# Kernel tuning notes

Hardware: AMD Instinct MI355X
Metric: run time of the kernel (lower is better)

The kernel has to match this reference:

```python
import jax, jax.numpy as jnp
import numpy as np

B_, K_, D_, L_, N_, R_ = 4, 4, 96, 2048, 16, 6
C_ = R_ + 2 * N_  # 38


def setup_inputs() -> dict:
    key = jax.random.key(0)
    ks = jax.random.split(key, 6)
    scale = 0.05  # keep projections in a realistic range (like 1/sqrt(fan_in) init)
    return {
        "xs": jax.random.normal(ks[0], (B_, K_, D_, L_), dtype=jnp.float32),
        "A_logs": jax.random.uniform(ks[1], (K_ * D_, N_), dtype=jnp.float32),
        "Ds": jax.random.normal(ks[2], (K_ * D_,), dtype=jnp.float32),
        "dt_projs_weight": jax.random.normal(ks[3], (K_, D_, R_), dtype=jnp.float32) * scale,
        "dt_projs_bias": jax.random.normal(ks[4], (K_, D_), dtype=jnp.float32) * scale,
        "x_proj_weight": jax.random.normal(ks[5], (K_, C_, D_), dtype=jnp.float32) * scale,
    }


def reference(xs, A_logs, Ds, dt_projs_weight, dt_projs_bias, x_proj_weight):
    B, K, D, L = xs.shape
    N = A_logs.shape[1]
    R = dt_projs_weight.shape[2]

    xs = xs.astype(jnp.float32)  # force_fp32=True

    # project x -> (delta, B, C):  [B,K,C,L]
    x_dbl = jnp.einsum("bkdl,kcd->bkcl", xs, x_proj_weight)
    dts, Bs, Cs = x_dbl[:, :, :R], x_dbl[:, :, R:R + N], x_dbl[:, :, R + N:]
    # dt low-rank -> per-channel delta: [B,K,D,L]
    dts = jnp.einsum("bkrl,kdr->bkdl", dts, dt_projs_weight)

    A = -jnp.exp(A_logs.astype(jnp.float32)).reshape(K, D, N)  # [K,D,N]
    Dskd = Ds.astype(jnp.float32).reshape(K, D)

    # delta_softplus with delta_bias
    delta = jax.nn.softplus(dts + dt_projs_bias.astype(jnp.float32)[None, :, :, None])

    # discretization: deltaA [B,K,D,L,N], deltaB_u [B,K,D,L,N]
    dA = jnp.exp(delta[..., None] * A[None, :, :, None, :])
    dBu = jnp.einsum("bkdl,bknl,bkdl->bkdln", delta, Bs, xs)

    # linear recurrence h_t = dA_t * h_{t-1} + dBu_t via parallel associative scan over L
    def combine(e1, e2):
        a1, b1 = e1
        a2, b2 = e2
        return a1 * a2, a2 * b1 + b2

    _, hs = jax.lax.associative_scan(combine, (dA, dBu), axis=3)  # hs: [B,K,D,L,N]

    # y_t = C_t . h_t + D * x_t
    y = jnp.einsum("bkdln,bknl->bkdl", hs, Cs) + Dskd[None, :, :, None] * xs
    return y.astype(jnp.float32)  # [B,K,D,L]
```

## Files before the change

kernel.cpp:

```cpp
#include <hip/hip_runtime.h>
#include <hip/hip_fp16.h>
#include <math.h>

#define B_ 4
#define K_ 4
#define D_ 96
#define L_ 2048
#define N_ 16
#define R_ 6
#define C_ 38

__device__ __forceinline__ float softplus_f(float x) {
    return fmaxf(x, 0.f) + __logf(1.f + __expf(-fabsf(x)));
}

#if __has_builtin(__builtin_amdgcn_exp2f)
__device__ __forceinline__ float exp2_fast(float x) { return __builtin_amdgcn_exp2f(x); }
#else
__device__ __forceinline__ float exp2_fast(float x) { return __expf(0.6931471805599453f * x); }
#endif

__device__ __forceinline__ float h2f(const uint4& v, int e) {
    return __half2float(((const __half*)&v)[e]);
}


__global__ __launch_bounds__(256) void proj_kernel(
    const float* __restrict__ xs, const float* __restrict__ xpw,
    uint4* __restrict__ BCc, float* __restrict__ dts_ws)
{
    __shared__ float sWt[D_][24];
    const int bk = blockIdx.x;
    const int k = bk & 3;
    const int cg = blockIdx.z;
    const int tid = threadIdx.x;
    const int c0 = (cg == 0) ? 0 : (R_ + N_);
    const int nr = (cg == 0) ? 22 : 16;

    for (int i = tid; i < nr * D_; i += 256) {
        const int r = i / D_, dd = i % D_;
        sWt[dd][r] = xpw[(k * C_ + c0 + r) * D_ + dd];
    }
    __syncthreads();

    const int l = blockIdx.y * 256 + tid;
    const float* Xl = xs + (size_t)bk * D_ * L_ + l;
    const int i8 = l & 7, t8 = l >> 3;
    uint4* BCb = BCc + ((size_t)bk * 8 + i8) * 4 * 256 + t8;

    if (cg == 0) {
        float acc[22];
#pragma unroll
        for (int r = 0; r < 22; ++r) acc[r] = 0.f;
#pragma unroll
        for (int d = 0; d < D_; ++d) {
            const float xv = Xl[d * L_];
            float wv[24];
#pragma unroll
            for (int q = 0; q < 6; ++q)
                *(float4*)&wv[q * 4] = *(const float4*)&sWt[d][q * 4];
#pragma unroll
            for (int r = 0; r < 22; ++r) acc[r] = fmaf(wv[r], xv, acc[r]);
        }
#pragma unroll
        for (int r = 0; r < R_; ++r)
            dts_ws[((size_t)bk * R_ + r) * L_ + l] = acc[r];
        union { __half h[8]; uint4 v; } p0, p1;
#pragma unroll
        for (int e = 0; e < 8; ++e) {
            p0.h[e] = __float2half(acc[6 + e]);
            p1.h[e] = __float2half(acc[14 + e]);
        }
        BCb[0 * 256] = p0.v;
        BCb[1 * 256] = p1.v;
    } else {
        float acc[16];
#pragma unroll
        for (int r = 0; r < 16; ++r) acc[r] = 0.f;
#pragma unroll
        for (int d = 0; d < D_; ++d) {
            const float xv = Xl[d * L_];
            float wv[16];
#pragma unroll
            for (int q = 0; q < 4; ++q)
                *(float4*)&wv[q * 4] = *(const float4*)&sWt[d][q * 4];
#pragma unroll
            for (int r = 0; r < 16; ++r) acc[r] = fmaf(wv[r], xv, acc[r]);
        }
        union { __half h[8]; uint4 v; } p0, p1;
#pragma unroll
        for (int e = 0; e < 8; ++e) {
            p0.h[e] = __float2half(acc[e]);
            p1.h[e] = __float2half(acc[8 + e]);
        }
        BCb[2 * 256] = p0.v;
        BCb[3 * 256] = p1.v;
    }
}

__global__ __launch_bounds__(512) void scan_kernel(
    const float* __restrict__ xs, const float* __restrict__ A_logs,
    const float* __restrict__ Ds, const float* __restrict__ dtw,
    const float* __restrict__ dtb, const float* __restrict__ dts_ws,
    const uint4* __restrict__ BCc, float* __restrict__ out)
{
    __shared__ float sAw[8][8];
    __shared__ float sBw[8][8];
    __shared__ float sy[256][9];

    const int bkd = blockIdx.x;
    const int d = bkd % D_;
    const int bk = bkd / D_;
    const int k = bk & 3;
    const int kd = k * D_ + d;
    const int tid = threadIdx.x;
    const int g = tid >> 8;
    const int t = tid & 255;
    const int lane = tid & 63;
    const int gw = tid >> 6;

    const uint4* BC = BCc + (size_t)bk * 8 * 4 * 256;
    const int jB = g, jC = 2 + g;

    const float4* xv4 = (const float4*)(xs + (size_t)bkd * L_);
    const float4 xa = xv4[t * 2], xb = xv4[t * 2 + 1];
    float x[8] = {xa.x, xa.y, xa.z, xa.w, xb.x, xb.y, xb.z, xb.w};

    float del[8];
    const float bias = dtb[kd];
#pragma unroll
    for (int j = 0; j < 8; ++j) del[j] = bias;
    const float* w2 = dtw + (size_t)kd * R_;
    const float4* dts4 = (const float4*)(dts_ws + (size_t)bk * R_ * L_);
#pragma unroll
    for (int r = 0; r < R_; ++r) {
        const float wr = w2[r];
        const float4 t0 = dts4[r * (L_ / 4) + t * 2];
        const float4 t1 = dts4[r * (L_ / 4) + t * 2 + 1];
        del[0] = fmaf(wr, t0.x, del[0]); del[1] = fmaf(wr, t0.y, del[1]);
        del[2] = fmaf(wr, t0.z, del[2]); del[3] = fmaf(wr, t0.w, del[3]);
        del[4] = fmaf(wr, t1.x, del[4]); del[5] = fmaf(wr, t1.y, del[5]);
        del[6] = fmaf(wr, t1.z, del[6]); del[7] = fmaf(wr, t1.w, del[7]);
    }
#pragma unroll
    for (int j = 0; j < 8; ++j) del[j] = softplus_f(del[j]);

    float A2[8];
    const float* Ap = A_logs + (size_t)kd * N_ + g * 8;
#pragma unroll
    for (int n = 0; n < 8; ++n) A2[n] = -__expf(Ap[n]) * 1.44269504f;
    const float Dval = Ds[kd];

    float a[8], b[8];
#pragma unroll
    for (int n = 0; n < 8; ++n) { a[n] = 1.f; b[n] = 0.f; }
#pragma unroll
    for (int i = 0; i < 8; ++i) {
        const uint4 cB = BC[(i * 4 + jB) * 256 + t];
        const float dl = del[i];
        const float dx = dl * x[i];
#pragma unroll
        for (int n = 0; n < 8; ++n) {
            const float dA = exp2_fast(dl * A2[n]);
            b[n] = fmaf(dA, b[n], dx * h2f(cB, n));
            a[n] *= dA;
        }
    }

#pragma unroll
    for (int off = 1; off < 64; off <<= 1) {
#pragma unroll
        for (int n = 0; n < 8; ++n) {
            const float pa = __shfl_up(a[n], off, 64);
            const float pb = __shfl_up(b[n], off, 64);
            if (lane >= off) {
                b[n] = fmaf(a[n], pb, b[n]);
                a[n] *= pa;
            }
        }
    }
    if (lane == 63) {
#pragma unroll
        for (int n = 0; n < 8; ++n) { sAw[gw][n] = a[n]; sBw[gw][n] = b[n]; }
    }
    __syncthreads();

    float h[8];
#pragma unroll
    for (int n = 0; n < 8; ++n) {
        float ae = __shfl_up(a[n], 1, 64);
        float be = __shfl_up(b[n], 1, 64);
        if (lane == 0) { ae = 1.f; be = 0.f; }
        float wb = 0.f;
        for (int w = g * 4; w < gw; ++w) wb = fmaf(sAw[w][n], wb, sBw[w][n]);
        h[n] = fmaf(ae, wb, be);
    }

    float yv[8];
#pragma unroll
    for (int j = 0; j < 8; ++j) yv[j] = (g == 0) ? Dval * x[j] : 0.f;
#pragma unroll
    for (int i = 0; i < 8; ++i) {
        const uint4 cB = BC[(i * 4 + jB) * 256 + t];
        const uint4 cC = BC[(i * 4 + jC) * 256 + t];
        const float dl = del[i];
        const float dx = dl * x[i];
        float y = yv[i];
#pragma unroll
        for (int n = 0; n < 8; ++n) {
            const float dA = exp2_fast(dl * A2[n]);
            h[n] = fmaf(dA, h[n], dx * h2f(cB, n));
            y = fmaf(h[n], h2f(cC, n), y);
        }
        yv[i] = y;
    }

    if (g == 1) {
#pragma unroll
        for (int j = 0; j < 8; ++j) sy[t][j] = yv[j];
    }
    __syncthreads();
    if (g == 0) {
#pragma unroll
        for (int j = 0; j < 8; ++j) yv[j] += sy[t][j];
        float4* ov = (float4*)(out + (size_t)bkd * L_);
        ov[t * 2]     = make_float4(yv[0], yv[1], yv[2], yv[3]);
        ov[t * 2 + 1] = make_float4(yv[4], yv[5], yv[6], yv[7]);
    }
}

extern "C" void kernel_launch(void* const* d_in, const int* in_sizes, int n_in,
                              void* d_out, int out_size, void* d_ws, size_t ws_size,
                              hipStream_t stream) {
    const float* xs = (const float*)d_in[0];
    const float* A_logs = (const float*)d_in[1];
    const float* Ds = (const float*)d_in[2];
    const float* dtw = (const float*)d_in[3];
    const float* dtb = (const float*)d_in[4];
    const float* xpw = (const float*)d_in[5];
    float* out = (float*)d_out;

    uint4* BCc = (uint4*)d_ws;
    float* dts_ws = (float*)(BCc + (size_t)B_ * K_ * 8 * 4 * 256);

    proj_kernel<<<dim3(B_ * K_, 8, 2), 256, 0, stream>>>(xs, xpw, BCc, dts_ws);
    scan_kernel<<<B_ * K_ * D_, 512, 0, stream>>>(
        xs, A_logs, Ds, dtw, dtb, dts_ws, BCc, out);
}
```

Baseline: 132.4 us.

## Split projection into five uniform 8-row groups and prefetch B/C in scan

The projection kernel now uses five z-slices of 8 output rows each (four B/C groups plus a zero-padded dt group) instead of two unbalanced slices of 22 and 16 rows. This raises the block count from 256 to 640 and cuts per-thread register use, at the cost of re-reading xs more times. The scan kernel also software-prefetches the fp16 B/C packets two iterations ahead in both passes, so global load latency overlaps with the exp/fma work.

```diff
diff --git a/kernel.cpp b/kernel.cpp
--- a/kernel.cpp
+++ b/kernel.cpp
@@ -29,72 +29,48 @@
     const float* __restrict__ xs, const float* __restrict__ xpw,
     uint4* __restrict__ BCc, float* __restrict__ dts_ws)
 {
-    __shared__ float sWt[D_][24];
+    __shared__ float sWt[D_][8];
     const int bk = blockIdx.x;
     const int k = bk & 3;
     const int cg = blockIdx.z;
     const int tid = threadIdx.x;
-    const int c0 = (cg == 0) ? 0 : (R_ + N_);
-    const int nr = (cg == 0) ? 22 : 16;
-
-    for (int i = tid; i < nr * D_; i += 256) {
+    const int c0 = (cg < 4) ? (R_ + cg * 8) : 0;
+    const int nr = (cg < 4) ? 8 : R_;
+
+    for (int i = tid; i < 8 * D_; i += 256) {
         const int r = i / D_, dd = i % D_;
-        sWt[dd][r] = xpw[(k * C_ + c0 + r) * D_ + dd];
+        sWt[dd][r] = (r < nr) ? xpw[(k * C_ + c0 + r) * D_ + dd] : 0.f;
     }
     __syncthreads();
 
     const int l = blockIdx.y * 256 + tid;
     const float* Xl = xs + (size_t)bk * D_ * L_ + l;
-    const int i8 = l & 7, t8 = l >> 3;
-    uint4* BCb = BCc + ((size_t)bk * 8 + i8) * 4 * 256 + t8;
-
-    if (cg == 0) {
-        float acc[22];
-#pragma unroll
-        for (int r = 0; r < 22; ++r) acc[r] = 0.f;
-#pragma unroll
-        for (int d = 0; d < D_; ++d) {
-            const float xv = Xl[d * L_];
-            float wv[24];
-#pragma unroll
-            for (int q = 0; q < 6; ++q)
-                *(float4*)&wv[q * 4] = *(const float4*)&sWt[d][q * 4];
-#pragma unroll
-            for (int r = 0; r < 22; ++r) acc[r] = fmaf(wv[r], xv, acc[r]);
-        }
+
+    float acc[8];
+#pragma unroll
+    for (int r = 0; r < 8; ++r) acc[r] = 0.f;
+
+#pragma unroll
+    for (int d = 0; d < D_; ++d) {
+        const float xv = Xl[d * L_];
+        float4 w0 = *(const float4*)&sWt[d][0];
+        float4 w1 = *(const float4*)&sWt[d][4];
+        acc[0] = fmaf(w0.x, xv, acc[0]); acc[1] = fmaf(w0.y, xv, acc[1]);
+        acc[2] = fmaf(w0.z, xv, acc[2]); acc[3] = fmaf(w0.w, xv, acc[3]);
+        acc[4] = fmaf(w1.x, xv, acc[4]); acc[5] = fmaf(w1.y, xv, acc[5]);
+        acc[6] = fmaf(w1.z, xv, acc[6]); acc[7] = fmaf(w1.w, xv, acc[7]);
+    }
+
+    if (cg < 4) {
+        const int i8 = l & 7, t8 = l >> 3;
+        union { __half h[8]; uint4 v; } p;
+#pragma unroll
+        for (int e = 0; e < 8; ++e) p.h[e] = __float2half(acc[e]);
+        BCc[(((size_t)bk * 8 + i8) * 4 + cg) * 256 + t8] = p.v;
+    } else {
 #pragma unroll
         for (int r = 0; r < R_; ++r)
             dts_ws[((size_t)bk * R_ + r) * L_ + l] = acc[r];
-        union { __half h[8]; uint4 v; } p0, p1;
-#pragma unroll
-        for (int e = 0; e < 8; ++e) {
-            p0.h[e] = __float2half(acc[6 + e]);
-            p1.h[e] = __float2half(acc[14 + e]);
-        }
-        BCb[0 * 256] = p0.v;
-        BCb[1 * 256] = p1.v;
-    } else {
-        float acc[16];
-#pragma unroll
-        for (int r = 0; r < 16; ++r) acc[r] = 0.f;
-#pragma unroll
-        for (int d = 0; d < D_; ++d) {
-            const float xv = Xl[d * L_];
-            float wv[16];
-#pragma unroll
-            for (int q = 0; q < 4; ++q)
-                *(float4*)&wv[q * 4] = *(const float4*)&sWt[d][q * 4];
-#pragma unroll
-            for (int r = 0; r < 16; ++r) acc[r] = fmaf(wv[r], xv, acc[r]);
-        }
-        union { __half h[8]; uint4 v; } p0, p1;
-#pragma unroll
-        for (int e = 0; e < 8; ++e) {
-            p0.h[e] = __float2half(acc[e]);
-            p1.h[e] = __float2half(acc[8 + e]);
-        }
-        BCb[2 * 256] = p0.v;
-        BCb[3 * 256] = p1.v;
     }
 }
 
@@ -126,6 +102,10 @@
     const float4 xa = xv4[t * 2], xb = xv4[t * 2 + 1];
     float x[8] = {xa.x, xa.y, xa.z, xa.w, xb.x, xb.y, xb.z, xb.w};
 
+    uint4 qB[2];
+    qB[0] = BC[(0 * 4 + jB) * 256 + t];
+    qB[1] = BC[(1 * 4 + jB) * 256 + t];
+
     float del[8];
     const float bias = dtb[kd];
 #pragma unroll
@@ -156,7 +136,8 @@
     for (int n = 0; n < 8; ++n) { a[n] = 1.f; b[n] = 0.f; }
 #pragma unroll
     for (int i = 0; i < 8; ++i) {
-        const uint4 cB = BC[(i * 4 + jB) * 256 + t];
+        const uint4 cB = qB[i & 1];
+        if (i < 6) qB[i & 1] = BC[((i + 2) * 4 + jB) * 256 + t];
         const float dl = del[i];
         const float dx = dl * x[i];
 #pragma unroll
@@ -166,6 +147,12 @@
             a[n] *= dA;
         }
     }
+
+    uint4 pB[2], pC[2];
+    pB[0] = BC[(0 * 4 + jB) * 256 + t];
+    pC[0] = BC[(0 * 4 + jC) * 256 + t];
+    pB[1] = BC[(1 * 4 + jB) * 256 + t];
+    pC[1] = BC[(1 * 4 + jC) * 256 + t];
 
 #pragma unroll
     for (int off = 1; off < 64; off <<= 1) {
@@ -201,8 +188,12 @@
     for (int j = 0; j < 8; ++j) yv[j] = (g == 0) ? Dval * x[j] : 0.f;
 #pragma unroll
     for (int i = 0; i < 8; ++i) {
-        const uint4 cB = BC[(i * 4 + jB) * 256 + t];
-        const uint4 cC = BC[(i * 4 + jC) * 256 + t];
+        const uint4 cB = pB[i & 1];
+        const uint4 cC = pC[i & 1];
+        if (i < 6) {
+            pB[i & 1] = BC[((i + 2) * 4 + jB) * 256 + t];
+            pC[i & 1] = BC[((i + 2) * 4 + jC) * 256 + t];
+        }
         const float dl = del[i];
         const float dx = dl * x[i];
         float y = yv[i];
@@ -243,7 +234,7 @@
     uint4* BCc = (uint4*)d_ws;
     float* dts_ws = (float*)(BCc + (size_t)B_ * K_ * 8 * 4 * 256);
 
-    proj_kernel<<<dim3(B_ * K_, 8, 2), 256, 0, stream>>>(xs, xpw, BCc, dts_ws);
+    proj_kernel<<<dim3(B_ * K_, 8, 5), 256, 0, stream>>>(xs, xpw, BCc, dts_ws);
     scan_kernel<<<B_ * K_ * D_, 512, 0, stream>>>(
         xs, A_logs, Ds, dtw, dtb, dts_ws, BCc, out);
 }
```

Result: slower. 139.3 us (+5.2%).
